# Kernel optimization log

Measured on AMD Instinct MI355X. Metric: run time of the kernel, lower is better.

## Reference

```python
import jax, jax.numpy as jnp
import numpy as np

EPS = 1e-12

def _l2norm(v, axis):
    n = jnp.sqrt(jnp.sum(v * v, axis=axis, keepdims=True))
    return v / jnp.maximum(n, EPS)

def setup_inputs() -> dict:
    key = jax.random.key(0)
    k1, k2, k3, k4 = jax.random.split(key, 4)
    N, T, D, K = 8, 2048, 512, 64
    x = jax.random.normal(k1, (N, T, D), dtype=jnp.float32)
    W = jax.random.normal(k2, (K, D), dtype=jnp.float32) * (1.0 / np.sqrt(D))  # Conv1d(k=1) weight squeezed
    b = jax.random.normal(k3, (K,), dtype=jnp.float32) * 0.01
    centroids = jax.random.uniform(k4, (K, D), dtype=jnp.float32)
    return {"x": x, "W": W, "b": b, "centroids": centroids}

def reference(x, W, b, centroids):
    N, T, D = x.shape
    K = centroids.shape[0]
    # L2-normalize descriptors along feature dim
    xn = _l2norm(x, axis=2)                                  # [N,T,D]
    # Conv1d with kernel_size=1 == per-timestep linear: [N,K,T] logits over clusters
    logits = jnp.einsum('ntd,kd->nkt', xn, W) + b[None, :, None]
    a = jax.nn.softmax(logits, axis=1)                       # soft assignment over K
    # Algebraically equal to sum_t a[n,k,t] * (xn[n,t,:] - c[k,:])
    vlad = jnp.einsum('nkt,ntd->nkd', a, xn) \
         - jnp.sum(a, axis=2)[:, :, None] * centroids[None]  # [N,K,D]
    vlad = _l2norm(vlad, axis=2)                             # intra-normalize per cluster
    vlad = vlad.reshape(N, K * D)
    return _l2norm(vlad, axis=1)                             # global L2 normalize
```

## Files before the change

kernel.cpp:

```cpp
#include <hip/hip_runtime.h>
#include <math.h>

#define EPS 1e-12f
#define NN 8
#define TT 2048
#define DD 512
#define KK 64

typedef short short8 __attribute__((ext_vector_type(8)));
typedef float floatx4 __attribute__((ext_vector_type(4)));

__device__ __forceinline__ unsigned short f2bf(float f) {
    unsigned int u = __float_as_uint(f);
    u += 0x7FFFu + ((u >> 16) & 1u);
    return (unsigned short)(u >> 16);
}
__device__ __forceinline__ unsigned int pack2(float a, float b) {
    return (unsigned int)f2bf(a) | ((unsigned int)f2bf(b) << 16);
}
__device__ __forceinline__ float bf2f_lo(unsigned int u) {
    return __uint_as_float(u << 16);
}
__device__ __forceinline__ float bf2f_hi(unsigned int u) {
    return __uint_as_float(u & 0xFFFF0000u);
}


__global__ __launch_bounds__(256) void kA(const float* __restrict__ x,
                                          const float* __restrict__ W,
                                          const float* __restrict__ bias,
                                          unsigned short* __restrict__ xb,
                                          unsigned short* __restrict__ aTs,
                                          float* __restrict__ asumP) {
    __shared__ unsigned short sW[32768];
    __shared__ float sRed[256];

    const int tid = threadIdx.x;

    const int w = tid >> 6, lane = tid & 63;
    const int l = lane & 15, q = lane >> 4;
    const int row0 = blockIdx.x * 64 + w * 16;
    const int row = row0 + l;
    const int n = row0 >> 11;
    const int tl0 = row0 & (TT - 1);

    const float* xr = x + (size_t)row * DD;
    unsigned short* xo = xb + (size_t)row * DD;
    short8 fragA[16];
    float ssq = 0.0f;
#pragma unroll
    for (int s = 0; s < 16; ++s) {
        float4 u0 = *(const float4*)(xr + s * 32 + q * 8);
        float4 u1 = *(const float4*)(xr + s * 32 + q * 8 + 4);
        ssq += u0.x*u0.x + u0.y*u0.y + u0.z*u0.z + u0.w*u0.w
             + u1.x*u1.x + u1.y*u1.y + u1.z*u1.z + u1.w*u1.w;
        uint4 pk;
        pk.x = pack2(u0.x, u0.y); pk.y = pack2(u0.z, u0.w);
        pk.z = pack2(u1.x, u1.y); pk.w = pack2(u1.z, u1.w);
        union { uint4 u; short8 s8; } cvt; cvt.u = pk;
        fragA[s] = cvt.s8;
        *(uint4*)(xo + s * 32 + q * 8) = pk;
    }

    {
        const int sp = tid >> 4, hp = (tid >> 2) & 3, qp = tid & 3;
        const float* wsrc = W + (size_t)(hp * 16) * DD + sp * 32 + qp * 8;
        unsigned short* wdst = sW + (size_t)tid * 128;
#pragma unroll
        for (int j = 0; j < 16; ++j) {
            float4 u0 = *(const float4*)(wsrc + (size_t)j * DD);
            float4 u1 = *(const float4*)(wsrc + (size_t)j * DD + 4);
            uint4 pk;
            pk.x = pack2(u0.x, u0.y); pk.y = pack2(u0.z, u0.w);
            pk.z = pack2(u1.x, u1.y); pk.w = pack2(u1.z, u1.w);
            *(uint4*)(wdst + j * 8) = pk;
        }
    }

    ssq += __shfl_xor(ssq, 16, 64);
    ssq += __shfl_xor(ssq, 32, 64);
    float st = 1.0f / fmaxf(sqrtf(ssq), EPS);

    __syncthreads();

    floatx4 acc[4];
#pragma unroll
    for (int h = 0; h < 4; ++h) acc[h] = floatx4{0.f, 0.f, 0.f, 0.f};
#pragma unroll
    for (int s = 0; s < 16; ++s) {
#pragma unroll
        for (int h = 0; h < 4; ++h) {
            short8 wf = *(const short8*)(sW + ((size_t)((s * 4 + h) * 64) + lane) * 8);
            acc[h] = __builtin_amdgcn_mfma_f32_16x16x32_bf16(fragA[s], wf, acc[h], 0, 0, 0);
        }
    }

    float sr[4];
#pragma unroll
    for (int r = 0; r < 4; ++r) sr[r] = __shfl(st, 4 * q + r, 64);
    float bj[4];
#pragma unroll
    for (int h = 0; h < 4; ++h) bj[h] = bias[h * 16 + l];

    float av[4][4];
#pragma unroll
    for (int r = 0; r < 4; ++r) {
        float v0 = acc[0][r] * sr[r] + bj[0], v1 = acc[1][r] * sr[r] + bj[1];
        float v2 = acc[2][r] * sr[r] + bj[2], v3 = acc[3][r] * sr[r] + bj[3];
        float m = fmaxf(fmaxf(v0, v1), fmaxf(v2, v3));
#pragma unroll
        for (int msk = 1; msk <= 8; msk <<= 1) m = fmaxf(m, __shfl_xor(m, msk, 64));
        float e0 = __expf(v0 - m), e1 = __expf(v1 - m), e2 = __expf(v2 - m), e3 = __expf(v3 - m);
        float ss = e0 + e1 + e2 + e3;
#pragma unroll
        for (int msk = 1; msk <= 8; msk <<= 1) ss += __shfl_xor(ss, msk, 64);
        float inv = 1.0f / ss;
        av[0][r] = e0 * inv; av[1][r] = e1 * inv; av[2][r] = e2 * inv; av[3][r] = e3 * inv;
    }

#pragma unroll
    for (int h = 0; h < 4; ++h) {
        uint2 p;
        p.x = pack2(av[h][0] * sr[0], av[h][1] * sr[1]);
        p.y = pack2(av[h][2] * sr[2], av[h][3] * sr[3]);
        *(uint2*)(aTs + ((size_t)(n * KK + h * 16 + l)) * TT + tl0 + 4 * q) = p;
    }

#pragma unroll
    for (int h = 0; h < 4; ++h) {
        float sh = av[h][0] + av[h][1] + av[h][2] + av[h][3];
        sh += __shfl_xor(sh, 16, 64);
        sh += __shfl_xor(sh, 32, 64);
        if (q == 0) sRed[w * 64 + h * 16 + l] = sh;
    }
    __syncthreads();
    if (tid < 64) {
        float s0 = sRed[tid] + sRed[64 + tid] + sRed[128 + tid] + sRed[192 + tid];
        asumP[(size_t)blockIdx.x * 64 + tid] = s0;
    }
}

__global__ __launch_bounds__(256) void kB(const unsigned short* __restrict__ xb,
                                          const unsigned short* __restrict__ aTs,
                                          unsigned short* __restrict__ part16) {
    __shared__ unsigned char smem[17408];
    unsigned short* sX0 = (unsigned short*)smem;
    unsigned short* sX1 = sX0 + 4096;
    float* sT = (float*)smem;

    const int tid = threadIdx.x;
    const int wv = tid >> 6, lane = tid & 63;
    const int l = lane & 15, q = lane >> 4;
    const int bid = blockIdx.x;
    const int low = bid & 63;
    const int n = low >> 3, tc = low & 7, dt = bid >> 6;

    const int ts = tid & 63, dq = tid >> 6;
    const unsigned short* xbase = xb + ((size_t)(n * TT + tc * 256)) * DD + dt * 64 + dq * 16;
    const int g = ts >> 3, t7 = ts & 7;

#define STAGE(S, BUF)                                                          \
    {                                                                          \
        const unsigned short* p_ = xbase + (size_t)((S) * 64 + ts) * DD;       \
        unsigned short vals[16];                                               \
        *(uint4*)(vals) = *(const uint4*)(p_);                                 \
        *(uint4*)(vals + 8) = *(const uint4*)(p_ + 8);                         \
        _Pragma("unroll")                                                      \
        for (int e = 0; e < 16; ++e) {                                         \
            int d_ = dq * 16 + e;                                              \
            (BUF)[d_ * 64 + ((g ^ (d_ & 7)) << 3) + t7] = vals[e];             \
        }                                                                      \
    }

    floatx4 acc[4];
#pragma unroll
    for (int nt = 0; nt < 4; ++nt) acc[nt] = floatx4{0.f, 0.f, 0.f, 0.f};
    const unsigned short* abase = aTs + ((size_t)(n * KK + wv * 16 + l)) * TT + tc * 256;

    STAGE(0, sX0);
    __syncthreads();
#pragma unroll
    for (int s = 0; s < 4; ++s) {
        unsigned short* cur = (s & 1) ? sX1 : sX0;
        unsigned short* nxt = (s & 1) ? sX0 : sX1;
        if (s < 3) {
            if (s == 0) STAGE(1, nxt)
            else if (s == 1) STAGE(2, nxt)
            else STAGE(3, nxt)
        }
#pragma unroll
        for (int kb = 0; kb < 2; ++kb) {
            short8 af = *(const short8*)(abase + s * 64 + kb * 32 + q * 8);
            int gg = q + 4 * kb;
#pragma unroll
            for (int nt = 0; nt < 4; ++nt) {
                int d = nt * 16 + l;
                short8 bf = *(const short8*)(cur + d * 64 + ((gg ^ (d & 7)) << 3));
                acc[nt] = __builtin_amdgcn_mfma_f32_16x16x32_bf16(af, bf, acc[nt], 0, 0, 0);
            }
        }
        __syncthreads();
    }
#undef STAGE

#pragma unroll
    for (int nt = 0; nt < 4; ++nt)
#pragma unroll
        for (int r = 0; r < 4; ++r)
            sT[(wv * 16 + 4 * q + r) * 68 + nt * 16 + l] = acc[nt][r];
    __syncthreads();

    unsigned short* pbase = part16 + ((size_t)(tc * 512 + n * KK)) * DD + dt * 64;
    const int fq = tid & 15, kr = tid >> 4;
#pragma unroll
    for (int i = 0; i < 4; ++i) {
        int k = i * 16 + kr;
        float4 val = *(float4*)(sT + k * 68 + fq * 4);
        uint2 o;
        o.x = pack2(val.x, val.y);
        o.y = pack2(val.z, val.w);
        *(uint2*)(pbase + (size_t)k * DD + fq * 4) = o;
    }
}

__global__ __launch_bounds__(128) void kC(const unsigned short* __restrict__ part16,
                                          const float* __restrict__ asumP,
                                          const float* __restrict__ cent,
                                          float* __restrict__ out) {
    __shared__ float red[2];
    __shared__ float sAsum;
    const int nk = blockIdx.x;
    const int n = nk >> 6, k = nk & 63;
    const int tid = threadIdx.x;

    if (tid < 32) {
        float p = asumP[(size_t)(n * 32 + tid) * 64 + k];
#pragma unroll
        for (int m = 16; m >= 1; m >>= 1) p += __shfl_xor(p, m, 64);
        if (tid == 0) sAsum = p;
    }
    __syncthreads();
    float as = sAsum;

    float4 cc = ((const float4*)(cent + (size_t)k * DD))[tid];
    float4 a4 = make_float4(-as * cc.x, -as * cc.y, -as * cc.z, -as * cc.w);
#pragma unroll
    for (int tc = 0; tc < 8; ++tc) {
        uint2 p = ((const uint2*)(part16 + ((size_t)(tc * 512 + nk)) * DD))[tid];
        a4.x += bf2f_lo(p.x); a4.y += bf2f_hi(p.x);
        a4.z += bf2f_lo(p.y); a4.w += bf2f_hi(p.y);
    }
    float ssq = a4.x*a4.x + a4.y*a4.y + a4.z*a4.z + a4.w*a4.w;
#pragma unroll
    for (int m = 32; m >= 1; m >>= 1) ssq += __shfl_xor(ssq, m, 64);
    if ((tid & 63) == 0) red[tid >> 6] = ssq;
    __syncthreads();
    float nr = sqrtf(red[0] + red[1]);
    float sc = 1.0f / (fmaxf(nr, EPS) * 8.0f);
    a4.x *= sc; a4.y *= sc; a4.z *= sc; a4.w *= sc;
    ((float4*)(out + (size_t)nk * DD))[tid] = a4;
}

extern "C" void kernel_launch(void* const* d_in, const int* in_sizes, int n_in,
                              void* d_out, int out_size, void* d_ws, size_t ws_size,
                              hipStream_t stream) {
    const float* x    = (const float*)d_in[0];
    const float* W    = (const float*)d_in[1];
    const float* b    = (const float*)d_in[2];
    const float* cent = (const float*)d_in[3];
    float* out = (float*)d_out;

    float* w = (float*)d_ws;
    unsigned short* xb     = (unsigned short*)(w + 0);
    unsigned short* aTs    = (unsigned short*)(w + 4194304);
    unsigned short* part16 = (unsigned short*)(w + 4718592);
    float* asumP = w + 5767168;

    hipLaunchKernelGGL(kA, dim3(256), dim3(256), 0, stream, x, W, b, xb, aTs, asumP);
    hipLaunchKernelGGL(kB, dim3(512), dim3(256), 0, stream, xb, aTs, part16);
    hipLaunchKernelGGL(kC, dim3(512), dim3(128), 0, stream, part16, asumP, cent, out);
}
```

Baseline: 94.16 us.

## Widen kA to 1024-thread blocks and halve kB's d-tile to double its grid

kA now runs 16 waves per 64-row block. Each wave does one 16x16 MFMA tile (row group by cluster group), with x staged into swizzled shared memory using coalesced float4 loads. Softmax over K is then reduced across waves through shared memory. kB's d-tile drops from 64 to 32 columns, doubling its grid to 1024 blocks and reducing shared memory per block. The aim is more parallelism and better latency hiding on both kernels, at the cost of extra shared-memory traffic, syncs and redundant A-fragment loads in kB.

After: 99.45 us. 5.6% more time.

```diff
diff --git a/kernel.cpp b/kernel.cpp
--- a/kernel.cpp
+++ b/kernel.cpp
@@ -26,116 +26,124 @@
 }
 
 
-__global__ __launch_bounds__(256) void kA(const float* __restrict__ x,
-                                          const float* __restrict__ W,
-                                          const float* __restrict__ bias,
-                                          unsigned short* __restrict__ xb,
-                                          unsigned short* __restrict__ aTs,
-                                          float* __restrict__ asumP) {
+__global__ __launch_bounds__(1024) void kA(const float* __restrict__ x,
+                                           const float* __restrict__ W,
+                                           const float* __restrict__ bias,
+                                           unsigned short* __restrict__ xb,
+                                           unsigned short* __restrict__ aTs,
+                                           float* __restrict__ asumP) {
     __shared__ unsigned short sW[32768];
+    __shared__ unsigned short sX[32768];
+    __shared__ float sSt[64];
+    __shared__ float sM[4 * 64];
+    __shared__ float sS[4 * 64];
     __shared__ float sRed[256];
 
     const int tid = threadIdx.x;
-
     const int w = tid >> 6, lane = tid & 63;
     const int l = lane & 15, q = lane >> 4;
-    const int row0 = blockIdx.x * 64 + w * 16;
-    const int row = row0 + l;
+    const int row0 = blockIdx.x * 64;
     const int n = row0 >> 11;
     const int tl0 = row0 & (TT - 1);
 
-    const float* xr = x + (size_t)row * DD;
-    unsigned short* xo = xb + (size_t)row * DD;
-    short8 fragA[16];
-    float ssq = 0.0f;
-#pragma unroll
-    for (int s = 0; s < 16; ++s) {
-        float4 u0 = *(const float4*)(xr + s * 32 + q * 8);
-        float4 u1 = *(const float4*)(xr + s * 32 + q * 8 + 4);
-        ssq += u0.x*u0.x + u0.y*u0.y + u0.z*u0.z + u0.w*u0.w
-             + u1.x*u1.x + u1.y*u1.y + u1.z*u1.z + u1.w*u1.w;
+    float ssqr[4] = {0.f, 0.f, 0.f, 0.f};
+#pragma unroll
+    for (int i = 0; i < 8; ++i) {
+        const int rl = w * 4 + (i >> 1);
+        const int d0 = (i & 1) * 256 + lane * 4;
+        float4 u = *(const float4*)(x + (size_t)(row0 + rl) * DD + d0);
+        ssqr[i >> 1] += u.x * u.x + u.y * u.y + u.z * u.z + u.w * u.w;
+        uint2 pk;
+        pk.x = pack2(u.x, u.y);
+        pk.y = pack2(u.z, u.w);
+        *(uint2*)(xb + (size_t)(row0 + rl) * DD + d0) = pk;
+        const int s0 = d0 >> 5, q0 = (d0 >> 3) & 3, half = (d0 >> 2) & 1;
+        const int g0 = rl >> 4, lr = rl & 15;
+        const int slot = ((g0 * 16 + s0) * 4 + q0) * 16 + (lr ^ ((s0 * 4 + q0) & 15));
+        *(uint2*)(sX + slot * 8 + half * 4) = pk;
+    }
+
+#pragma unroll
+    for (int j = 0; j < 4; ++j) {
+        const int slot = tid * 4 + j;
+        const int lw = slot & 15, qw = (slot >> 4) & 3, hw = (slot >> 6) & 3, sw = slot >> 8;
+        const float* src = W + (size_t)(hw * 16 + lw) * DD + sw * 32 + qw * 8;
+        float4 u0 = *(const float4*)(src);
+        float4 u1 = *(const float4*)(src + 4);
         uint4 pk;
         pk.x = pack2(u0.x, u0.y); pk.y = pack2(u0.z, u0.w);
         pk.z = pack2(u1.x, u1.y); pk.w = pack2(u1.z, u1.w);
-        union { uint4 u; short8 s8; } cvt; cvt.u = pk;
-        fragA[s] = cvt.s8;
-        *(uint4*)(xo + s * 32 + q * 8) = pk;
+        const int sl2 = slot ^ ((slot >> 4) & 7);
+        *(uint4*)(sW + sl2 * 8) = pk;
+    }
+
+#pragma unroll
+    for (int rr = 0; rr < 4; ++rr) {
+        float ss = ssqr[rr];
+#pragma unroll
+        for (int m = 1; m <= 32; m <<= 1) ss += __shfl_xor(ss, m, 64);
+        if (lane == 0) sSt[w * 4 + rr] = 1.0f / fmaxf(sqrtf(ss), EPS);
+    }
+    __syncthreads();
+
+    const int g = w & 3, h = w >> 2;
+    floatx4 acc = floatx4{0.f, 0.f, 0.f, 0.f};
+#pragma unroll
+    for (int s = 0; s < 16; ++s) {
+        short8 af = *(const short8*)(sX + (((g * 16 + s) * 4 + q) * 16 + (l ^ ((s * 4 + q) & 15))) * 8);
+        const int slot = (s * 4 + h) * 64 + lane;
+        short8 wf = *(const short8*)(sW + (slot ^ ((slot >> 4) & 7)) * 8);
+        acc = __builtin_amdgcn_mfma_f32_16x16x32_bf16(af, wf, acc, 0, 0, 0);
+    }
+
+    const float bj = bias[h * 16 + l];
+    float sr[4], v[4];
+#pragma unroll
+    for (int r = 0; r < 4; ++r) {
+        sr[r] = sSt[g * 16 + 4 * q + r];
+        v[r] = acc[r] * sr[r] + bj;
+        float m = v[r];
+#pragma unroll
+        for (int msk = 1; msk <= 8; msk <<= 1) m = fmaxf(m, __shfl_xor(m, msk, 64));
+        if (l == 0) sM[h * 64 + g * 16 + 4 * q + r] = m;
+    }
+    __syncthreads();
+    float e[4];
+#pragma unroll
+    for (int r = 0; r < 4; ++r) {
+        const int t = g * 16 + 4 * q + r;
+        float M = fmaxf(fmaxf(sM[t], sM[64 + t]), fmaxf(sM[128 + t], sM[192 + t]));
+        e[r] = __expf(v[r] - M);
+        float ss = e[r];
+#pragma unroll
+        for (int msk = 1; msk <= 8; msk <<= 1) ss += __shfl_xor(ss, msk, 64);
+        if (l == 0) sS[h * 64 + t] = ss;
+    }
+    __syncthreads();
+    float a[4];
+#pragma unroll
+    for (int r = 0; r < 4; ++r) {
+        const int t = g * 16 + 4 * q + r;
+        float inv = 1.0f / (sS[t] + sS[64 + t] + sS[128 + t] + sS[192 + t]);
+        a[r] = e[r] * inv;
     }
 
     {
-        const int sp = tid >> 4, hp = (tid >> 2) & 3, qp = tid & 3;
-        const float* wsrc = W + (size_t)(hp * 16) * DD + sp * 32 + qp * 8;
-        unsigned short* wdst = sW + (size_t)tid * 128;
-#pragma unroll
-        for (int j = 0; j < 16; ++j) {
-            float4 u0 = *(const float4*)(wsrc + (size_t)j * DD);
-            float4 u1 = *(const float4*)(wsrc + (size_t)j * DD + 4);
-            uint4 pk;
-            pk.x = pack2(u0.x, u0.y); pk.y = pack2(u0.z, u0.w);
-            pk.z = pack2(u1.x, u1.y); pk.w = pack2(u1.z, u1.w);
-            *(uint4*)(wdst + j * 8) = pk;
-        }
-    }
-
-    ssq += __shfl_xor(ssq, 16, 64);
-    ssq += __shfl_xor(ssq, 32, 64);
-    float st = 1.0f / fmaxf(sqrtf(ssq), EPS);
-
-    __syncthreads();
-
-    floatx4 acc[4];
-#pragma unroll
-    for (int h = 0; h < 4; ++h) acc[h] = floatx4{0.f, 0.f, 0.f, 0.f};
-#pragma unroll
-    for (int s = 0; s < 16; ++s) {
-#pragma unroll
-        for (int h = 0; h < 4; ++h) {
-            short8 wf = *(const short8*)(sW + ((size_t)((s * 4 + h) * 64) + lane) * 8);
-            acc[h] = __builtin_amdgcn_mfma_f32_16x16x32_bf16(fragA[s], wf, acc[h], 0, 0, 0);
-        }
-    }
-
-    float sr[4];
-#pragma unroll
-    for (int r = 0; r < 4; ++r) sr[r] = __shfl(st, 4 * q + r, 64);
-    float bj[4];
-#pragma unroll
-    for (int h = 0; h < 4; ++h) bj[h] = bias[h * 16 + l];
-
-    float av[4][4];
-#pragma unroll
-    for (int r = 0; r < 4; ++r) {
-        float v0 = acc[0][r] * sr[r] + bj[0], v1 = acc[1][r] * sr[r] + bj[1];
-        float v2 = acc[2][r] * sr[r] + bj[2], v3 = acc[3][r] * sr[r] + bj[3];
-        float m = fmaxf(fmaxf(v0, v1), fmaxf(v2, v3));
-#pragma unroll
-        for (int msk = 1; msk <= 8; msk <<= 1) m = fmaxf(m, __shfl_xor(m, msk, 64));
-        float e0 = __expf(v0 - m), e1 = __expf(v1 - m), e2 = __expf(v2 - m), e3 = __expf(v3 - m);
-        float ss = e0 + e1 + e2 + e3;
-#pragma unroll
-        for (int msk = 1; msk <= 8; msk <<= 1) ss += __shfl_xor(ss, msk, 64);
-        float inv = 1.0f / ss;
-        av[0][r] = e0 * inv; av[1][r] = e1 * inv; av[2][r] = e2 * inv; av[3][r] = e3 * inv;
-    }
-
-#pragma unroll
-    for (int h = 0; h < 4; ++h) {
         uint2 p;
-        p.x = pack2(av[h][0] * sr[0], av[h][1] * sr[1]);
-        p.y = pack2(av[h][2] * sr[2], av[h][3] * sr[3]);
-        *(uint2*)(aTs + ((size_t)(n * KK + h * 16 + l)) * TT + tl0 + 4 * q) = p;
-    }
-
-#pragma unroll
-    for (int h = 0; h < 4; ++h) {
-        float sh = av[h][0] + av[h][1] + av[h][2] + av[h][3];
-        sh += __shfl_xor(sh, 16, 64);
-        sh += __shfl_xor(sh, 32, 64);
-        if (q == 0) sRed[w * 64 + h * 16 + l] = sh;
-    }
+        p.x = pack2(a[0] * sr[0], a[1] * sr[1]);
+        p.y = pack2(a[2] * sr[2], a[3] * sr[3]);
+        *(uint2*)(aTs + ((size_t)(n * KK + h * 16 + l)) * TT + tl0 + g * 16 + 4 * q) = p;
+    }
+
+    float sh = a[0] + a[1] + a[2] + a[3];
+    sh += __shfl_xor(sh, 16, 64);
+    sh += __shfl_xor(sh, 32, 64);
+    if (q == 0) sRed[w * 16 + l] = sh;
     __syncthreads();
     if (tid < 64) {
-        float s0 = sRed[tid] + sRed[64 + tid] + sRed[128 + tid] + sRed[192 + tid];
+        const int hh = tid >> 4, ll = tid & 15;
+        float s0 = sRed[(hh * 4 + 0) * 16 + ll] + sRed[(hh * 4 + 1) * 16 + ll]
+                 + sRed[(hh * 4 + 2) * 16 + ll] + sRed[(hh * 4 + 3) * 16 + ll];
         asumP[(size_t)blockIdx.x * 64 + tid] = s0;
     }
 }
@@ -143,9 +151,9 @@
 __global__ __launch_bounds__(256) void kB(const unsigned short* __restrict__ xb,
                                           const unsigned short* __restrict__ aTs,
                                           unsigned short* __restrict__ part16) {
-    __shared__ unsigned char smem[17408];
+    __shared__ unsigned char smem[9216];
     unsigned short* sX0 = (unsigned short*)smem;
-    unsigned short* sX1 = sX0 + 4096;
+    unsigned short* sX1 = sX0 + 2048;
     float* sT = (float*)smem;
 
     const int tid = threadIdx.x;
@@ -156,25 +164,24 @@
     const int n = low >> 3, tc = low & 7, dt = bid >> 6;
 
     const int ts = tid & 63, dq = tid >> 6;
-    const unsigned short* xbase = xb + ((size_t)(n * TT + tc * 256)) * DD + dt * 64 + dq * 16;
+    const unsigned short* xbase = xb + ((size_t)(n * TT + tc * 256)) * DD + dt * 32 + dq * 8;
     const int g = ts >> 3, t7 = ts & 7;
 
 #define STAGE(S, BUF)                                                          \
     {                                                                          \
         const unsigned short* p_ = xbase + (size_t)((S) * 64 + ts) * DD;       \
-        unsigned short vals[16];                                               \
+        unsigned short vals[8];                                                \
         *(uint4*)(vals) = *(const uint4*)(p_);                                 \
-        *(uint4*)(vals + 8) = *(const uint4*)(p_ + 8);                         \
         _Pragma("unroll")                                                      \
-        for (int e = 0; e < 16; ++e) {                                         \
-            int d_ = dq * 16 + e;                                              \
+        for (int e = 0; e < 8; ++e) {                                          \
+            int d_ = dq * 8 + e;                                               \
             (BUF)[d_ * 64 + ((g ^ (d_ & 7)) << 3) + t7] = vals[e];             \
         }                                                                      \
     }
 
-    floatx4 acc[4];
-#pragma unroll
-    for (int nt = 0; nt < 4; ++nt) acc[nt] = floatx4{0.f, 0.f, 0.f, 0.f};
+    floatx4 acc[2];
+    acc[0] = floatx4{0.f, 0.f, 0.f, 0.f};
+    acc[1] = floatx4{0.f, 0.f, 0.f, 0.f};
     const unsigned short* abase = aTs + ((size_t)(n * KK + wv * 16 + l)) * TT + tc * 256;
 
     STAGE(0, sX0);
@@ -193,7 +200,7 @@
             short8 af = *(const short8*)(abase + s * 64 + kb * 32 + q * 8);
             int gg = q + 4 * kb;
 #pragma unroll
-            for (int nt = 0; nt < 4; ++nt) {
+            for (int nt = 0; nt < 2; ++nt) {
                 int d = nt * 16 + l;
                 short8 bf = *(const short8*)(cur + d * 64 + ((gg ^ (d & 7)) << 3));
                 acc[nt] = __builtin_amdgcn_mfma_f32_16x16x32_bf16(af, bf, acc[nt], 0, 0, 0);
@@ -204,18 +211,18 @@
 #undef STAGE
 
 #pragma unroll
-    for (int nt = 0; nt < 4; ++nt)
+    for (int nt = 0; nt < 2; ++nt)
 #pragma unroll
         for (int r = 0; r < 4; ++r)
-            sT[(wv * 16 + 4 * q + r) * 68 + nt * 16 + l] = acc[nt][r];
-    __syncthreads();
-
-    unsigned short* pbase = part16 + ((size_t)(tc * 512 + n * KK)) * DD + dt * 64;
-    const int fq = tid & 15, kr = tid >> 4;
-#pragma unroll
-    for (int i = 0; i < 4; ++i) {
-        int k = i * 16 + kr;
-        float4 val = *(float4*)(sT + k * 68 + fq * 4);
+            sT[(wv * 16 + 4 * q + r) * 36 + nt * 16 + l] = acc[nt][r];
+    __syncthreads();
+
+    unsigned short* pbase = part16 + ((size_t)(tc * 512 + n * KK)) * DD + dt * 32;
+    const int fq = tid & 7, kr = tid >> 3;
+#pragma unroll
+    for (int i = 0; i < 2; ++i) {
+        int k = i * 32 + kr;
+        float4 val = *(float4*)(sT + k * 36 + fq * 4);
         uint2 o;
         o.x = pack2(val.x, val.y);
         o.y = pack2(val.z, val.w);
@@ -250,7 +257,7 @@
         a4.x += bf2f_lo(p.x); a4.y += bf2f_hi(p.x);
         a4.z += bf2f_lo(p.y); a4.w += bf2f_hi(p.y);
     }
-    float ssq = a4.x*a4.x + a4.y*a4.y + a4.z*a4.z + a4.w*a4.w;
+    float ssq = a4.x * a4.x + a4.y * a4.y + a4.z * a4.z + a4.w * a4.w;
 #pragma unroll
     for (int m = 32; m >= 1; m >>= 1) ssq += __shfl_xor(ssq, m, 64);
     if ((tid & 63) == 0) red[tid >> 6] = ssq;
@@ -276,7 +283,7 @@
     unsigned short* part16 = (unsigned short*)(w + 4718592);
     float* asumP = w + 5767168;
 
-    hipLaunchKernelGGL(kA, dim3(256), dim3(256), 0, stream, x, W, b, xb, aTs, asumP);
-    hipLaunchKernelGGL(kB, dim3(512), dim3(256), 0, stream, xb, aTs, part16);
+    hipLaunchKernelGGL(kA, dim3(256), dim3(1024), 0, stream, x, W, b, xb, aTs, asumP);
+    hipLaunchKernelGGL(kB, dim3(1024), dim3(256), 0, stream, xb, aTs, part16);
     hipLaunchKernelGGL(kC, dim3(512), dim3(128), 0, stream, part16, asumP, cent, out);
 }
```
